# Optimization experiments

Hardware: AMD Instinct MI355X
Metric: run time of the kernel (lower is better)

Reference implementation:

```python
import jax, jax.numpy as jnp
import numpy as np

DIM = 768
NUM_HEADS = 12
HEAD_DIM = DIM // NUM_HEADS
SCALE = HEAD_DIM ** -0.5


def setup_inputs() -> dict:
    key = jax.random.key(0)
    k1, k2, k3, k4 = jax.random.split(key, 4)
    B, N, C = 4, 2048, DIM
    x = jax.random.normal(k1, (B, N, C), dtype=jnp.float32)
    # nn.Linear(dim, 3*dim, bias=False): weight shape (3C, C), y = x @ W^T
    w_qkv = jax.random.normal(k2, (3 * C, C), dtype=jnp.float32) * (C ** -0.5)
    # nn.Linear(dim, dim) with default bias=True
    w_proj = jax.random.normal(k3, (C, C), dtype=jnp.float32) * (C ** -0.5)
    b_proj = jax.random.normal(k4, (C,), dtype=jnp.float32) * 0.02
    return {"x": x, "w_qkv": w_qkv, "w_proj": w_proj, "b_proj": b_proj}


def reference(x, w_qkv, w_proj, b_proj):
    B, N, C = x.shape
    H, D = NUM_HEADS, HEAD_DIM
    qkv = jnp.einsum('bnc,oc->bno', x, w_qkv)  # (B, N, 3C)
    qkv = qkv.reshape(B, N, 3, H, D).transpose(2, 0, 3, 1, 4)  # (3, B, H, N, D)
    q, k, v = qkv[0], qkv[1], qkv[2]
    attn = jnp.einsum('bhnd,bhmd->bhnm', q, k) * jnp.float32(SCALE)  # (B,H,N,N)
    attn = jax.nn.softmax(attn, axis=-1)
    out = jnp.einsum('bhnm,bhmd->bhnd', attn, v)  # (B,H,N,D)
    out = out.transpose(0, 2, 1, 3).reshape(B, N, C)
    out = jnp.einsum('bnc,oc->bno', out, w_proj) + b_proj
    return out
```

## Files before the change

### kernel.cpp

```cpp
#include <hip/hip_runtime.h>
#include <math.h>

#define B_ 4
#define N_ 2048
#define C_ 768
#define H_ 12
#define D_ 64
#define QKSCALE_ 0.18033688011112042f

typedef unsigned short u16;
typedef unsigned int u32;
typedef short s16x8 __attribute__((ext_vector_type(8)));
typedef float f32x4 __attribute__((ext_vector_type(4)));
typedef float f32x16 __attribute__((ext_vector_type(16)));

__device__ __forceinline__ u16 f2bf(float f) {
    union { float f; u32 u; } v; v.f = f;
    u32 r = (v.u + 0x7fffu + ((v.u >> 16) & 1u)) >> 16;
    return (u16)r;
}

__device__ __forceinline__ void gl_lds16(const u16* g, u16* l) {
    __builtin_amdgcn_global_load_lds(
        (__attribute__((address_space(1))) void*)g,
        (__attribute__((address_space(3))) void*)l, 16, 0, 0);
}

#define NX4_  (B_ * N_ * C_ / 4)
#define NWQ4_ (3 * C_ * C_ / 4)
#define NWP4_ (C_ * C_ / 4)
__global__ __launch_bounds__(256) void cvt_all(const float4* __restrict__ x,
                                               const float4* __restrict__ wq,
                                               const float4* __restrict__ wp,
                                               ushort4* __restrict__ xb,
                                               ushort4* __restrict__ wqb,
                                               ushort4* __restrict__ wpb)
{
    const int tot = NX4_ + NWQ4_ + NWP4_;
    int i = blockIdx.x * blockDim.x + threadIdx.x;
    const int stride = gridDim.x * blockDim.x;
    for (; i < tot; i += stride) {
        const float4* s; ushort4* d; int j;
        if (i < NX4_)              { s = x;  d = xb;  j = i; }
        else if (i < NX4_ + NWQ4_) { s = wq; d = wqb; j = i - NX4_; }
        else                       { s = wp; d = wpb; j = i - NX4_ - NWQ4_; }
        float4 v = s[j];
        ushort4 o;
        o.x = f2bf(v.x); o.y = f2bf(v.y); o.z = f2bf(v.z); o.w = f2bf(v.w);
        d[j] = o;
    }
}

template<int BM, int WPEU, bool OUT_BF16, bool BIAS, bool QSCALE>
__global__ __launch_bounds__(256, WPEU) void gemm_mfma(const u16* __restrict__ A,
                                                       const u16* __restrict__ Bm,
                                                       const float* __restrict__ bias,
                                                       void* __restrict__ Cout,
                                                       int M, int N, int K)
{
    constexpr int MF  = BM / 32;
    constexpr int AC  = BM / 32;
    constexpr int ASZ = BM * 64, BSZ = 128 * 64;
    __shared__ __align__(16) u16 As[2 * ASZ];
    __shared__ __align__(16) u16 Bs[2 * BSZ];
    const int tid  = threadIdx.x;
    const int wv   = tid >> 6;
    const int lane = tid & 63;
    const int lr   = lane & 15;
    const int lq   = lane >> 4;
    const int wm   = (wv >> 1) * (BM / 2);
    const int wn   = (wv & 1) * 64;
    const int row0 = blockIdx.y * BM, col0 = blockIdx.x * 128;

    f32x4 acc[MF][4];
    #pragma unroll
    for (int i = 0; i < MF; i++)
        #pragma unroll
        for (int j = 0; j < 4; j++) { f32x4 z = {0.f,0.f,0.f,0.f}; acc[i][j] = z; }

    const int srow   = lane >> 3;
    const int schunk = ((lane & 7) ^ srow) * 8;

    const int arow_base = (BM / 4) * wv;
    const u16* gA = A + (size_t)(row0 + arow_base + srow) * K + schunk;
    const u16* gB = Bm + (size_t)(col0 + 32 * wv + srow) * K + schunk;
    const int aoff = arow_base * 64;
    const int boff = (32 * wv) * 64;

    const int nIter = K / 64;

    #pragma unroll
    for (int c = 0; c < AC; c++)
        gl_lds16(gA + (size_t)(8 * c) * K, As + aoff + c * 8 * 64);
    #pragma unroll
    for (int c = 0; c < 4; c++)
        gl_lds16(gB + (size_t)(8 * c) * K, Bs + boff + c * 8 * 64);

    for (int t = 0; t < nIter; t++) {
        const int cur = t & 1;
        __syncthreads();
        if (t + 1 < nIter) {
            const int k1 = (t + 1) * 64;
            const int nb = cur ^ 1;
            #pragma unroll
            for (int c = 0; c < AC; c++)
                gl_lds16(gA + (size_t)(8 * c) * K + k1, As + nb * ASZ + aoff + c * 8 * 64);
            #pragma unroll
            for (int c = 0; c < 4; c++)
                gl_lds16(gB + (size_t)(8 * c) * K + k1, Bs + nb * BSZ + boff + c * 8 * 64);
        }
        const u16* __restrict__ Ac = As + cur * ASZ;
        const u16* __restrict__ Bc = Bs + cur * BSZ;
        #pragma unroll
        for (int kk = 0; kk < 2; kk++) {
            const int fo = ((4 * kk + lq) ^ (lr & 7)) * 8;
            s16x8 af[MF], bfr[4];
            #pragma unroll
            for (int i = 0; i < MF; i++)
                af[i] = *(const s16x8*)&Ac[(wm + 16*i + lr) * 64 + fo];
            #pragma unroll
            for (int j = 0; j < 4; j++)
                bfr[j] = *(const s16x8*)&Bc[(wn + 16*j + lr) * 64 + fo];
            #pragma unroll
            for (int i = 0; i < MF; i++)
                #pragma unroll
                for (int j = 0; j < 4; j++)
                    acc[i][j] = __builtin_amdgcn_mfma_f32_16x16x32_bf16(af[i], bfr[j], acc[i][j], 0, 0, 0);
        }
    }

    #pragma unroll
    for (int i = 0; i < MF; i++) {
        #pragma unroll
        for (int j = 0; j < 4; j++) {
            const int col = col0 + wn + 16*j + lr;
            float bv = BIAS ? bias[col] : 0.f;
            #pragma unroll
            for (int r = 0; r < 4; r++) {
                const int row = row0 + wm + 16*i + lq*4 + r;
                float v = acc[i][j][r] + bv;
                if (QSCALE && col < C_) v *= QKSCALE_;
                if (OUT_BF16) ((u16*)Cout)[(size_t)row * N + col] = f2bf(v);
                else          ((float*)Cout)[(size_t)row * N + col] = v;
            }
        }
    }
}

__global__ __launch_bounds__(256, 3) void attn_mfma(const u16* __restrict__ qkv,
                                                    u16* __restrict__ attout)
{
    __shared__ __align__(16) u16 Ks[2][64 * 64];
    __shared__ __align__(16) u16 Vt[2][64][72];

    const int tid  = threadIdx.x;
    const int wv   = tid >> 6;
    const int lane = tid & 63;
    const int l31  = lane & 31;
    const int hi   = lane >> 5;
    const int n0   = blockIdx.x * 128;
    const int bh   = blockIdx.y, b = bh / H_, h = bh % H_;
    const size_t rs = 3 * C_;

    const u16* Qg = qkv + ((size_t)b * N_ + n0) * rs + h * D_;
    const u16* Kg = qkv + ((size_t)b * N_) * rs + C_ + h * D_;
    const u16* Vg = Kg + C_;

    s16x8 qf[4];
    #pragma unroll
    for (int kk = 0; kk < 4; kk++)
        qf[kk] = *(const s16x8*)(Qg + (size_t)(32*wv + l31) * rs + kk*16 + hi*8);

    const f32x16 z16 = {0.f,0.f,0.f,0.f,0.f,0.f,0.f,0.f,
                        0.f,0.f,0.f,0.f,0.f,0.f,0.f,0.f};
    f32x16 oacc[2] = {z16, z16};
    float li = 0.f;

    const int skey = tid >> 2;
    const int sc0  = (tid & 3) * 2;
    const int scA  = (sc0     ^ (skey & 7)) * 8;
    const int scB  = ((sc0+1) ^ (skey & 7)) * 8;
    const int vc = tid & 7, vp = tid >> 3;
    const int vkey0 = 2 * vp, vd0 = vc * 8;
    const int vcol0 = (vkey0 + 8 * vc) & 63;

    s16x8 kr0, kr1, vr0, vr1;
    {
        const u16* kp = Kg + (size_t)skey * rs + sc0 * 8;
        kr0 = *(const s16x8*)kp; kr1 = *(const s16x8*)(kp + 8);
        const u16* vp2 = Vg + (size_t)vkey0 * rs + vd0;
        vr0 = *(const s16x8*)vp2; vr1 = *(const s16x8*)(vp2 + rs);
    }
    *(s16x8*)&Ks[0][skey * 64 + scA] = kr0;
    *(s16x8*)&Ks[0][skey * 64 + scB] = kr1;
    #pragma unroll
    for (int u = 0; u < 8; u++) {
        u32 pk = (u32)(u16)vr0[u] | ((u32)(u16)vr1[u] << 16);
        *(u32*)&Vt[0][vd0 + u][vcol0] = pk;
    }
    {
        const u16* kp = Kg + (size_t)(64 + skey) * rs + sc0 * 8;
        kr0 = *(const s16x8*)kp; kr1 = *(const s16x8*)(kp + 8);
        const u16* vp2 = Vg + (size_t)(64 + vkey0) * rs + vd0;
        vr0 = *(const s16x8*)vp2; vr1 = *(const s16x8*)(vp2 + rs);
    }

    const int NT = N_ / 64;
    for (int t = 0; t < NT; t++) {
        const int cur = t & 1, nxt = cur ^ 1;
        __syncthreads();
        if (t + 1 < NT) {
            *(s16x8*)&Ks[nxt][skey * 64 + scA] = kr0;
            *(s16x8*)&Ks[nxt][skey * 64 + scB] = kr1;
            #pragma unroll
            for (int u = 0; u < 8; u++) {
                u32 pk = (u32)(u16)vr0[u] | ((u32)(u16)vr1[u] << 16);
                *(u32*)&Vt[nxt][vd0 + u][vcol0] = pk;
            }
        }
        if (t + 2 < NT) {
            const u16* kp = Kg + (size_t)((t+2)*64 + skey) * rs + sc0 * 8;
            kr0 = *(const s16x8*)kp; kr1 = *(const s16x8*)(kp + 8);
            const u16* vp2 = Vg + (size_t)((t+2)*64 + vkey0) * rs + vd0;
            vr0 = *(const s16x8*)vp2; vr1 = *(const s16x8*)(vp2 + rs);
        }

        #define KF(j, kk) (*(const s16x8*)&Ks[cur][(32*(j) + l31) * 64 + \
                           ((2*(kk) + hi) ^ (l31 & 7)) * 8])
        f32x16 st0 = __builtin_amdgcn_mfma_f32_32x32x16_bf16(KF(0,0), qf[0], z16, 0, 0, 0);
        f32x16 st1 = __builtin_amdgcn_mfma_f32_32x32x16_bf16(KF(1,0), qf[0], z16, 0, 0, 0);
        #pragma unroll
        for (int kk = 1; kk < 4; kk++) {
            st0 = __builtin_amdgcn_mfma_f32_32x32x16_bf16(KF(0,kk), qf[kk], st0, 0, 0, 0);
            st1 = __builtin_amdgcn_mfma_f32_32x32x16_bf16(KF(1,kk), qf[kk], st1, 0, 0, 0);
        }
        #undef KF

        #pragma unroll
        for (int j = 0; j < 2; j++) {
            const f32x16 s = j ? st1 : st0;
            float p[16];
            #pragma unroll
            for (int r = 0; r < 16; r++) p[r] = __builtin_amdgcn_exp2f(s[r]);
            #pragma unroll
            for (int r = 0; r < 16; r += 4)
                li += (p[r] + p[r+1]) + (p[r+2] + p[r+3]);
            u32 w[4][2];
            #pragma unroll
            for (int m = 0; m < 4; m++) {
                asm("v_cvt_pk_bf16_f32 %0, %1, %2"
                    : "=v"(w[m][0]) : "v"(p[4*m+0]), "v"(p[4*m+1]));
                asm("v_cvt_pk_bf16_f32 %0, %1, %2"
                    : "=v"(w[m][1]) : "v"(p[4*m+2]), "v"(p[4*m+3]));
            }
            #pragma unroll
            for (int h2 = 0; h2 < 2; h2++) {
                asm("v_permlane32_swap_b32 %0, %1"
                    : "+v"(w[2*h2][0]), "+v"(w[2*h2+1][0]));
                asm("v_permlane32_swap_b32 %0, %1"
                    : "+v"(w[2*h2][1]), "+v"(w[2*h2+1][1]));
                const int sp = 2*j + h2;
                union { u32 uw[4]; s16x8 v; } pa;
                pa.uw[0] = w[2*h2][0];   pa.uw[1] = w[2*h2][1];
                pa.uw[2] = w[2*h2+1][0]; pa.uw[3] = w[2*h2+1][1];
                #pragma unroll
                for (int j2 = 0; j2 < 2; j2++) {
                    const int pb = (2*sp + hi + 4*j2 + (l31 >> 3)) & 7;
                    s16x8 vb = *(const s16x8*)&Vt[cur][32*j2 + l31][pb * 8];
                    oacc[j2] = __builtin_amdgcn_mfma_f32_32x32x16_bf16(pa.v, vb, oacc[j2], 0, 0, 0);
                }
            }
        }
    }

    li += __shfl_xor(li, 32);
    const float inv = 1.f / li;
    #pragma unroll
    for (int r = 0; r < 16; r++) {
        const int qr = (r & 3) + 8 * (r >> 2) + 4 * hi;
        const float iv = __shfl(inv, qr);
        const size_t grow = (size_t)(b * N_ + n0 + 32*wv + qr);
        #pragma unroll
        for (int j2 = 0; j2 < 2; j2++)
            attout[grow * C_ + h * D_ + 32*j2 + l31] = f2bf(oacc[j2][r] * iv);
    }
}

extern "C" void kernel_launch(void* const* d_in, const int* in_sizes, int n_in,
                              void* d_out, int out_size, void* d_ws, size_t ws_size,
                              hipStream_t stream) {
    const float* x      = (const float*)d_in[0];
    const float* w_qkv  = (const float*)d_in[1];
    const float* w_proj = (const float*)d_in[2];
    const float* b_proj = (const float*)d_in[3];
    float* out = (float*)d_out;

    const int NX   = B_ * N_ * C_;
    const int NWQ  = 3 * C_ * C_;
    const int NWP  = C_ * C_;
    const int NQKV = B_ * N_ * 3 * C_;

    u16* xb   = (u16*)d_ws;
    u16* wqb  = xb + NX;
    u16* wpb  = wqb + NWQ;
    u16* qkvb = wpb + NWP;
    u16* attb = qkvb + NQKV;

    dim3 blk(256);

    cvt_all<<<768, blk, 0, stream>>>((const float4*)x, (const float4*)w_qkv,
                                     (const float4*)w_proj,
                                     (ushort4*)xb, (ushort4*)wqb, (ushort4*)wpb);

    const int M = B_ * N_;
    gemm_mfma<128, 2, true, false, true><<<dim3((3*C_)/128, M/128), blk, 0, stream>>>(
        xb, wqb, nullptr, qkvb, M, 3*C_, C_);

    attn_mfma<<<dim3(N_/128, B_ * H_), blk, 0, stream>>>(qkvb, attb);

    gemm_mfma<64, 3, false, true, false><<<dim3(C_/128, M/64), blk, 0, stream>>>(
        attb, wpb, b_proj, out, M, C_, C_);
}
```

Baseline: 210.7 us.

## Load K tiles via direct global-to-LDS, remap workgroups, raise MFMA priority

K tiles now go straight from global memory into LDS with global_load_lds, with the swizzle applied on the source address, instead of being staged through registers. This frees VGPRs and removes the LDS store instructions. Workgroup IDs are remapped so that consecutive blocks spread across heads and batches, which can change L2 and XCD locality of the K/V reads. s_setprio is raised around the MFMA sections so compute-phase waves are favoured over loads. The direct-to-LDS load relies on the existing __syncthreads and on vmcnt waits for ordering, so there is some risk that a tile is read before its load has landed.

```diff
diff --git a/kernel.cpp b/kernel.cpp
--- a/kernel.cpp
+++ b/kernel.cpp
@@ -158,8 +158,12 @@
     const int lane = tid & 63;
     const int l31  = lane & 31;
     const int hi   = lane >> 5;
-    const int n0   = blockIdx.x * 128;
-    const int bh   = blockIdx.y, b = bh / H_, h = bh % H_;
+
+    const int wgid = blockIdx.y * gridDim.x + blockIdx.x;
+    const int ix   = wgid >> 3;
+    const int bh   = (wgid & 7) * 6 + (ix >> 4);
+    const int n0   = (ix & 15) * 128;
+    const int b = bh / H_, h = bh % H_;
     const size_t rs = 3 * C_;
 
     const u16* Qg = qkv + ((size_t)b * N_ + n0) * rs + h * D_;
@@ -176,31 +180,27 @@
     f32x16 oacc[2] = {z16, z16};
     float li = 0.f;
 
-    const int skey = tid >> 2;
-    const int sc0  = (tid & 3) * 2;
-    const int scA  = (sc0     ^ (skey & 7)) * 8;
-    const int scB  = ((sc0+1) ^ (skey & 7)) * 8;
+    const int kkey = lane >> 3;
+    const u16* Kg_l = Kg + (size_t)(16*wv + kkey) * rs + ((lane & 7) ^ kkey) * 8;
+
     const int vc = tid & 7, vp = tid >> 3;
     const int vkey0 = 2 * vp, vd0 = vc * 8;
     const int vcol0 = (vkey0 + 8 * vc) & 63;
 
-    s16x8 kr0, kr1, vr0, vr1;
+    gl_lds16(Kg_l,                    &Ks[0][(16*wv) * 64]);
+    gl_lds16(Kg_l + (size_t)8 * rs,   &Ks[0][(16*wv + 8) * 64]);
+
+    s16x8 vr0, vr1;
     {
-        const u16* kp = Kg + (size_t)skey * rs + sc0 * 8;
-        kr0 = *(const s16x8*)kp; kr1 = *(const s16x8*)(kp + 8);
         const u16* vp2 = Vg + (size_t)vkey0 * rs + vd0;
         vr0 = *(const s16x8*)vp2; vr1 = *(const s16x8*)(vp2 + rs);
     }
-    *(s16x8*)&Ks[0][skey * 64 + scA] = kr0;
-    *(s16x8*)&Ks[0][skey * 64 + scB] = kr1;
     #pragma unroll
     for (int u = 0; u < 8; u++) {
         u32 pk = (u32)(u16)vr0[u] | ((u32)(u16)vr1[u] << 16);
         *(u32*)&Vt[0][vd0 + u][vcol0] = pk;
     }
     {
-        const u16* kp = Kg + (size_t)(64 + skey) * rs + sc0 * 8;
-        kr0 = *(const s16x8*)kp; kr1 = *(const s16x8*)(kp + 8);
         const u16* vp2 = Vg + (size_t)(64 + vkey0) * rs + vd0;
         vr0 = *(const s16x8*)vp2; vr1 = *(const s16x8*)(vp2 + rs);
     }
@@ -210,8 +210,9 @@
         const int cur = t & 1, nxt = cur ^ 1;
         __syncthreads();
         if (t + 1 < NT) {
-            *(s16x8*)&Ks[nxt][skey * 64 + scA] = kr0;
-            *(s16x8*)&Ks[nxt][skey * 64 + scB] = kr1;
+            const size_t ko = (size_t)(t + 1) * 64 * rs;
+            gl_lds16(Kg_l + ko,                  &Ks[nxt][(16*wv) * 64]);
+            gl_lds16(Kg_l + ko + (size_t)8 * rs, &Ks[nxt][(16*wv + 8) * 64]);
             #pragma unroll
             for (int u = 0; u < 8; u++) {
                 u32 pk = (u32)(u16)vr0[u] | ((u32)(u16)vr1[u] << 16);
@@ -219,14 +220,13 @@
             }
         }
         if (t + 2 < NT) {
-            const u16* kp = Kg + (size_t)((t+2)*64 + skey) * rs + sc0 * 8;
-            kr0 = *(const s16x8*)kp; kr1 = *(const s16x8*)(kp + 8);
             const u16* vp2 = Vg + (size_t)((t+2)*64 + vkey0) * rs + vd0;
             vr0 = *(const s16x8*)vp2; vr1 = *(const s16x8*)(vp2 + rs);
         }
 
         #define KF(j, kk) (*(const s16x8*)&Ks[cur][(32*(j) + l31) * 64 + \
                            ((2*(kk) + hi) ^ (l31 & 7)) * 8])
+        __builtin_amdgcn_s_setprio(1);
         f32x16 st0 = __builtin_amdgcn_mfma_f32_32x32x16_bf16(KF(0,0), qf[0], z16, 0, 0, 0);
         f32x16 st1 = __builtin_amdgcn_mfma_f32_32x32x16_bf16(KF(1,0), qf[0], z16, 0, 0, 0);
         #pragma unroll
@@ -234,6 +234,7 @@
             st0 = __builtin_amdgcn_mfma_f32_32x32x16_bf16(KF(0,kk), qf[kk], st0, 0, 0, 0);
             st1 = __builtin_amdgcn_mfma_f32_32x32x16_bf16(KF(1,kk), qf[kk], st1, 0, 0, 0);
         }
+        __builtin_amdgcn_s_setprio(0);
         #undef KF
 
         #pragma unroll
@@ -263,12 +264,14 @@
                 union { u32 uw[4]; s16x8 v; } pa;
                 pa.uw[0] = w[2*h2][0];   pa.uw[1] = w[2*h2][1];
                 pa.uw[2] = w[2*h2+1][0]; pa.uw[3] = w[2*h2+1][1];
+                __builtin_amdgcn_s_setprio(1);
                 #pragma unroll
                 for (int j2 = 0; j2 < 2; j2++) {
                     const int pb = (2*sp + hi + 4*j2 + (l31 >> 3)) & 7;
                     s16x8 vb = *(const s16x8*)&Vt[cur][32*j2 + l31][pb * 8];
                     oacc[j2] = __builtin_amdgcn_mfma_f32_32x32x16_bf16(pa.v, vb, oacc[j2], 0, 0, 0);
                 }
+                __builtin_amdgcn_s_setprio(0);
             }
         }
     }
```

Result: slower. 218.7 us (+3.8%).
